# Optimization experiments

Hardware: AMD Instinct MI355X
Metric: run time of the kernel (lower is better)

The kernel has to match this reference:

```python
import jax, jax.numpy as jnp
import numpy as np

K = 3          # kernel size
SH, SW = 2, 1  # stride
PH, PW = 1, 1  # padding


def conv2d(x, w, b, stride, pad):
    y = jax.lax.conv_general_dilated(
        x, w, window_strides=stride,
        padding=[(pad[0], pad[0]), (pad[1], pad[1])],
        dimension_numbers=('NCHW', 'OIHW', 'NCHW'))
    return y + b[None, :, None, None]


def setup_inputs() -> dict:
    key = jax.random.key(0)
    ks = jax.random.split(key, 4)
    x = jax.random.normal(ks[0], (8, 64, 128, 128), jnp.float32)
    # scale offset weights small so sampled offsets are O(1) pixels (exercises
    # the bilinear path without sampling far out of bounds)
    w_offset = jax.random.normal(ks[1], (18, 64, 3, 3), jnp.float32) * 0.02
    b_offset = jnp.zeros((18,), jnp.float32)
    w_mask = jax.random.normal(ks[2], (9, 64, 3, 3), jnp.float32) * 0.05
    b_mask = jnp.zeros((9,), jnp.float32)
    w_conv = jax.random.normal(ks[3], (64, 64, 3, 3), jnp.float32) * (1.0 / 24.0)
    return dict(x=x, w_offset=w_offset, b_offset=b_offset,
                w_mask=w_mask, b_mask=b_mask, w_conv=w_conv)


def _bilinear_gather(x, py, px):
    # x: [B,C,H,W]; py, px: [B,K2,Ho,Wo] float sampling coordinates.
    # Zero-padding outside the image (torchvision deform_conv2d semantics).
    B, C, H, W = x.shape
    y0f = jnp.floor(py)
    x0f = jnp.floor(px)
    dy = py - y0f
    dx = px - x0f
    y0 = y0f.astype(jnp.int32)
    x0 = x0f.astype(jnp.int32)

    def corner(yi, xi, wgt):
        valid = (yi >= 0) & (yi < H) & (xi >= 0) & (xi < W)
        yc = jnp.clip(yi, 0, H - 1)
        xc = jnp.clip(xi, 0, W - 1)
        # per-batch fancy gather -> [B, C, K2, Ho, Wo]
        g = jax.vmap(lambda xb, yb, xbi: xb[:, yb, xbi])(x, yc, xc)
        return g * (wgt * valid)[:, None]

    return (corner(y0,     x0,     (1 - dy) * (1 - dx))
            + corner(y0,     x0 + 1, (1 - dy) * dx)
            + corner(y0 + 1, x0,     dy * (1 - dx))
            + corner(y0 + 1, x0 + 1, dy * dx))


def reference(x, w_offset, b_offset, w_mask, b_mask, w_conv):
    B, C, H, W = x.shape
    offset = conv2d(x, w_offset, b_offset, (SH, SW), (PH, PW))   # [B, 2*K2, Ho, Wo]
    mask = jax.nn.sigmoid(conv2d(x, w_mask, b_mask, (SH, SW), (PH, PW)))  # [B, K2, Ho, Wo]
    Ho, Wo = offset.shape[2], offset.shape[3]
    K2 = K * K
    off = offset.reshape(B, K2, 2, Ho, Wo)
    off_y = off[:, :, 0]   # [B,K2,Ho,Wo]
    off_x = off[:, :, 1]
    ky = (jnp.arange(K2) // K).astype(jnp.float32)
    kx = (jnp.arange(K2) % K).astype(jnp.float32)
    hs = (jnp.arange(Ho) * SH - PH).astype(jnp.float32)
    ws = (jnp.arange(Wo) * SW - PW).astype(jnp.float32)
    py = off_y + ky[None, :, None, None] + hs[None, None, :, None]
    px = off_x + kx[None, :, None, None] + ws[None, None, None, :]
    sampled = _bilinear_gather(x, py, px) * mask[:, None]  # [B,C,K2,Ho,Wo]
    # weighted accumulate over in-channels and kernel taps
    out = jnp.einsum('ock,bckhw->bohw', w_conv.reshape(-1, C, K2), sampled)
    return out
```

## Files before the change

### kernel.cpp

```cpp
#include <hip/hip_runtime.h>
#include <hip/hip_fp16.h>
#include <math.h>

#define BB 8
#define CC 64
#define HH 128
#define WW 128
#define HO 64
#define WO 128
#define OC 64
#define HW (HH * WW)

typedef __attribute__((ext_vector_type(4))) float floatx4;
typedef __attribute__((ext_vector_type(8))) _Float16 half8;

__device__ __forceinline__ unsigned short f2h(float f) {
    __half h = __float2half(f);
    return __builtin_bit_cast(unsigned short, h);
}
__device__ __forceinline__ unsigned int packpair(float a, float b) {
    __half2 h = __floats2half2_rn(a, b);
    return __builtin_bit_cast(unsigned int, h);
}
__device__ __forceinline__ void wave_fence() {
    asm volatile("s_waitcnt lgkmcnt(0)" ::: "memory");
}

__global__ __launch_bounds__(256) void prep(
    const float* __restrict__ x,
    const float* __restrict__ w_off, const float* __restrict__ w_msk,
    const float* __restrict__ w_conv,
    unsigned int* __restrict__ xP,
    unsigned short* __restrict__ Wom, unsigned short* __restrict__ W2)
{
    __shared__ float T[66][65];
    int tid = threadIdx.x, bx = blockIdx.x;
    if (bx < 2048) {
        int wh = bx & 1, b = (bx >> 1) & 7, y = bx >> 4;
        int w0 = wh << 6;
        const float* xb = x + (((size_t)b * CC) * HH + y) * WW + w0;
#pragma unroll
        for (int i = 0; i < 4; ++i) {
            int idx = i * 256 + tid;
            int cch = idx >> 4, f4 = (idx & 15) << 2;
            floatx4 v = *(const floatx4*)(xb + (size_t)cch * HW + f4);
            T[f4 + 0][cch] = v.x;
            T[f4 + 1][cch] = v.y;
            T[f4 + 2][cch] = v.z;
            T[f4 + 3][cch] = v.w;
        }
        if (tid < 64) {
            float e = 0.0f;
            if (w0 + 64 < WW) e = xb[(size_t)tid * HW + 64];
            T[64][tid] = e;
        }
        __syncthreads();
        int c4 = tid & 15;
        int wr = tid >> 4;
        size_t rowbase = (((size_t)b * HH + y) * WW) + w0;
#pragma unroll
        for (int j = 0; j < 4; ++j) {
            int w = 16 * j + wr;
            floatx4 a  = *(const floatx4*)&T[w][4 * c4];
            floatx4 bb = *(const floatx4*)&T[w + 1][4 * c4];
            uint4 d;
            d.x = packpair(a.x, bb.x);
            d.y = packpair(a.y, bb.y);
            d.z = packpair(a.z, bb.z);
            d.w = packpair(a.w, bb.w);
            *(uint4*)(xP + (rowbase + w) * 64 + 4 * c4) = d;
        }
    } else if (bx < 2120) {
        int i = (bx - 2048) * 256 + tid;
        int chn = i / 576, kk = i % 576;
        int xs = kk >> 6, cc = kk & 63;
        float v = 0.0f;
        if (chn < 18)      v = w_off[(chn * CC + cc) * 9 + xs];
        else if (chn < 27) v = w_msk[((chn - 18) * CC + cc) * 9 + xs];
        Wom[i] = f2h(v);
    } else {
        int i = (bx - 2120) * 256 + tid;
        int k = i % 9, cc = (i / 9) % CC, o = i / (CC * 9);
        W2[((size_t)k * OC + o) * CC + cc] = f2h(w_conv[i]);
    }
}

__global__ __launch_bounds__(256) void fused(
    const unsigned int* __restrict__ xP,
    const unsigned short* __restrict__ Wom, const unsigned short* __restrict__ W2,
    const float* __restrict__ b_off, const float* __restrict__ b_msk,
    float* __restrict__ out)
{
    __shared__ __align__(16) char lds[38912];
    int tid = threadIdx.x;
    int lane = tid & 63;
    int wv = __builtin_amdgcn_readfirstlane(tid >> 6);
    char* wb = lds + wv * 9728;
    _Float16* XsH = (_Float16*)wb;
    float* omr = (float*)(wb + 7776);
    uint2* metaRw = (uint2*)wb;
    uint2* metaCw = (uint2*)(wb + 1152);
    char* Sw = wb + 2304;

    int g = blockIdx.x * 4 + wv;
    int b = g >> 9;
    int rem = g & 511;
    int h = rem >> 3;
    int w0 = (rem & 7) << 4;
    int h2 = 2 * h - 1;
    int m16 = lane & 15, q = lane >> 4;

    const unsigned int* xPb_u = xP + (size_t)b * HW * 64;

    for (int u = lane; u < 864; u += 64) {
        int ky = u / 288;
        int rm = u - ky * 288;
        int col = rm >> 4, c4 = rm & 15;
        int hy = h2 + ky, wc = w0 - 1 + col;
        unsigned int lo0 = 0u, lo1 = 0u;
        if ((unsigned)hy < (unsigned)HH && (unsigned)wc < (unsigned)WW) {
            const uint4 gg = *(const uint4*)(xPb_u + ((size_t)hy * WW + wc) * 64 + c4 * 4);
            lo0 = (gg.x & 0xffffu) | (gg.y << 16);
            lo1 = (gg.z & 0xffffu) | (gg.w << 16);
        }
        *(uint2*)(XsH + (ky * 18 + col) * 72 + c4 * 4) = make_uint2(lo0, lo1);
    }
    wave_fence();

    {
        floatx4 a0 = (floatx4){0.f, 0.f, 0.f, 0.f};
        floatx4 a1 = (floatx4){0.f, 0.f, 0.f, 0.f};
        const _Float16* wa0 = (const _Float16*)Wom + m16 * 576 + q * 8;
        const _Float16* wa1 = wa0 + 16 * 576;
#pragma unroll
        for (int t = 0; t < 18; ++t) {
            int xs = t >> 1, ky = xs / 3, kx = xs % 3;
            half8 bf = *(const half8*)(XsH + (ky * 18 + m16 + kx) * 72
                                       + (t & 1) * 32 + q * 8);
            half8 af0 = *(const half8*)(wa0 + t * 32);
            half8 af1 = *(const half8*)(wa1 + t * 32);
            a0 = __builtin_amdgcn_mfma_f32_16x16x32_f16(af0, bf, a0, 0, 0, 0);
            a1 = __builtin_amdgcn_mfma_f32_16x16x32_f16(af1, bf, a1, 0, 0, 0);
        }
#pragma unroll
        for (int r = 0; r < 4; ++r) {
            int c0 = q * 4 + r;
            omr[c0 * 17 + m16] = a0[r];
            if (c0 + 16 < 27) omr[(c0 + 16) * 17 + m16] = a1[r];
        }
    }
    wave_fence();

    for (int u = lane; u < 144; u += 64) {
        int kk = u >> 4, pos = u & 15;
        float offy = omr[(2 * kk) * 17 + pos] + b_off[2 * kk];
        float offx = omr[(2 * kk + 1) * 17 + pos] + b_off[2 * kk + 1];
        float mk = 1.0f / (1.0f + __expf(-(omr[(18 + kk) * 17 + pos] + b_msk[kk])));
        float py = offy + (float)(kk / 3) + (float)h2;
        float px = offx + (float)(kk % 3) + (float)(w0 + pos - 1);

        float y0f = floorf(py), x0f = floorf(px);
        float dy = py - y0f, dx = px - x0f;
        int y0 = (int)y0f, x0 = (int)x0f;
        int y1 = y0 + 1, x1 = x0 + 1;
        bool vy0 = (unsigned)y0 < (unsigned)HH;
        bool vy1 = (unsigned)y1 < (unsigned)HH;
        bool vx0 = (unsigned)x0 < (unsigned)WW;
        bool vx1 = (unsigned)x1 < (unsigned)WW;
        float w00 = (1.0f - dy) * (1.0f - dx) * ((vy0 && vx0) ? mk : 0.0f);
        float w01 = (1.0f - dy) * dx          * ((vy0 && vx1) ? mk : 0.0f);
        float w10 = dy * (1.0f - dx)          * ((vy1 && vx0) ? mk : 0.0f);
        float w11 = dy * dx                   * ((vy1 && vx1) ? mk : 0.0f);
        int xbase = min(max(x0, 0), WW - 2);
        bool s0 = x0 > xbase;
        bool s1 = x1 > xbase;
        float cxA = (s0 ? 0.f : w00) + (s1 ? 0.f : w01);
        float cyA = (s0 ? w00 : 0.f) + (s1 ? w01 : 0.f);
        float cxB = (s0 ? 0.f : w10) + (s1 ? 0.f : w11);
        float cyB = (s0 ? w10 : 0.f) + (s1 ? w11 : 0.f);
        int yc0 = min(max(y0, 0), HH - 1);
        int yc1 = min(max(y1, 0), HH - 1);

        __half2 hA = __floats2half2_rn(cxA, cyA);
        __half2 hB = __floats2half2_rn(cxB, cyB);
        metaCw[u] = make_uint2(__builtin_bit_cast(unsigned int, hA),
                               __builtin_bit_cast(unsigned int, hB));
        metaRw[u] = make_uint2((unsigned)(yc0 * WW + xbase) * 256u,
                               (unsigned)(yc1 * WW + xbase) * 256u);
    }
    wave_fence();

    int p = lane & 31;
    int ph4 = (lane >> 5) << 2;
    unsigned int voffC = 8u * (unsigned)p;
    const char* xPb = (const char*)xPb_u;

    floatx4 acc[4];
#pragma unroll
    for (int m = 0; m < 4; ++m) acc[m] = (floatx4){0.f, 0.f, 0.f, 0.f};

    half8 A[8];
    uint2 Ga0[4], Ga1[4], Gb0[4], Gb1[4];

    auto loadA = [&](int k) {
#pragma unroll
        for (int m = 0; m < 4; ++m)
#pragma unroll
            for (int ks = 0; ks < 2; ++ks)
                A[m * 2 + ks] = *(const half8*)((const _Float16*)W2
                    + ((size_t)(k * OC + m * 16 + m16)) * CC + ks * 32 + q * 8);
    };
    auto issueG = [&](int hhk, uint2 (&G0)[4], uint2 (&G1)[4]) {
        int k = hhk >> 1;
#pragma unroll
        for (int i = 0; i < 4; ++i) {
            int rw = ((hhk & 1) << 3) + ph4 + i;
            uint2 zw = metaRw[k * 16 + rw];
            G0[i] = *(const uint2*)(xPb + (zw.x + voffC));
            G1[i] = *(const uint2*)(xPb + (zw.y + voffC));
        }
    };
    auto blend = [&](int hhk, uint2 (&G0)[4], uint2 (&G1)[4]) {
        int k = hhk >> 1;
#pragma unroll
        for (int i = 0; i < 4; ++i) {
            int rw = ((hhk & 1) << 3) + ph4 + i;
            uint2 cf = metaCw[k * 16 + rw];
            __half2 hA = __builtin_bit_cast(__half2, cf.x);
            __half2 hB = __builtin_bit_cast(__half2, cf.y);
            __half2 t0 = __hfma2(hA, __builtin_bit_cast(__half2, G0[i].x),
                                 __hmul2(hB, __builtin_bit_cast(__half2, G1[i].x)));
            __half2 t1 = __hfma2(hA, __builtin_bit_cast(__half2, G0[i].y),
                                 __hmul2(hB, __builtin_bit_cast(__half2, G1[i].y)));
            __half v0 = __hadd(__low2half(t0), __high2half(t0));
            __half v1 = __hadd(__low2half(t1), __high2half(t1));
            unsigned int d = (unsigned int)__builtin_bit_cast(unsigned short, v0)
                           | ((unsigned int)__builtin_bit_cast(unsigned short, v1) << 16);
            *(unsigned int*)(Sw + rw * 128
                + (((p >> 2) ^ (rw & 7)) * 16 + (p & 3) * 4)) = d;
        }
    };
    auto mfma_tap = [&]() {
        half8 Bf0 = *(const half8*)(Sw + m16 * 128 + ((q ^ (m16 & 7)) * 16));
        half8 Bf1 = *(const half8*)(Sw + m16 * 128 + (((4 + q) ^ (m16 & 7)) * 16));
#pragma unroll
        for (int m = 0; m < 4; ++m) {
            acc[m] = __builtin_amdgcn_mfma_f32_16x16x32_f16(A[m * 2 + 0], Bf0, acc[m], 0, 0, 0);
            acc[m] = __builtin_amdgcn_mfma_f32_16x16x32_f16(A[m * 2 + 1], Bf1, acc[m], 0, 0, 0);
        }
    };

    loadA(0);
    issueG(0, Ga0, Ga1);
#pragma unroll 1
    for (int hh = 0; hh < 18; ++hh) {
        if (hh < 17) {
            if ((hh & 1) == 0) issueG(hh + 1, Gb0, Gb1);
            else               issueG(hh + 1, Ga0, Ga1);
        }
        __builtin_amdgcn_sched_barrier(0);
        if ((hh & 1) == 0) blend(hh, Ga0, Ga1);
        else               blend(hh, Gb0, Gb1);
        if (hh & 1) {
            wave_fence();
            mfma_tap();
            if (hh < 17) loadA((hh >> 1) + 1);
            __builtin_amdgcn_sched_barrier(0);
        }
    }

#pragma unroll
    for (int m = 0; m < 4; ++m)
#pragma unroll
        for (int r = 0; r < 4; ++r) {
            int o = m * 16 + q * 4 + r;
            out[(((size_t)b * OC + o) * HO + h) * WO + w0 + m16] = acc[m][r];
        }
}

extern "C" void kernel_launch(void* const* d_in, const int* in_sizes, int n_in,
                              void* d_out, int out_size, void* d_ws, size_t ws_size,
                              hipStream_t stream)
{
    const float* x      = (const float*)d_in[0];
    const float* w_off  = (const float*)d_in[1];
    const float* b_off  = (const float*)d_in[2];
    const float* w_msk  = (const float*)d_in[3];
    const float* b_msk  = (const float*)d_in[4];
    const float* w_conv = (const float*)d_in[5];
    float* out = (float*)d_out;

    unsigned int* xP = (unsigned int*)d_ws;
    unsigned short* Wom = (unsigned short*)(xP + (size_t)BB * HW * 64);
    unsigned short* W2 = Wom + 32 * 576;

    prep<<<dim3(2264), dim3(256), 0, stream>>>(x, w_off, w_msk, w_conv,
                                               xP, Wom, W2);
    fused<<<dim3(1024), dim3(256), 0, stream>>>(xP, Wom, W2,
                                                b_off, b_msk, out);
}
```

Measured before the change: 168.1 us.

## Use zero-padded NHWC fp16 layout and read offset-conv inputs directly from global

The prep kernel now writes x as a zero-padded (130x130) channel-last fp16 image instead of the paired-column packed layout, halving the intermediate size. The fused kernel drops the per-wave LDS staging of the 3x18 input tile and loads offset-conv operands straight from global memory, relying on padding to remove bounds checks. The bilinear gather now issues four separate corner loads with duplicated half2 coefficients, and the block-to-tile mapping is reordered so batches interleave. Together these cut LDS use and the workspace footprint, at the cost of more, smaller global loads in the gather loop.

```diff
diff --git a/kernel.cpp b/kernel.cpp
--- a/kernel.cpp
+++ b/kernel.cpp
@@ -10,6 +10,9 @@
 #define WO 128
 #define OC 64
 #define HW (HH * WW)
+#define PR 130
+#define PC 130
+#define PLH (PR * PC * 64)
 
 typedef __attribute__((ext_vector_type(4))) float floatx4;
 typedef __attribute__((ext_vector_type(8))) _Float16 half8;
@@ -18,8 +21,12 @@
     __half h = __float2half(f);
     return __builtin_bit_cast(unsigned short, h);
 }
-__device__ __forceinline__ unsigned int packpair(float a, float b) {
+__device__ __forceinline__ unsigned int pack2(float a, float b) {
     __half2 h = __floats2half2_rn(a, b);
+    return __builtin_bit_cast(unsigned int, h);
+}
+__device__ __forceinline__ unsigned int dup2(float a) {
+    __half2 h = __floats2half2_rn(a, a);
     return __builtin_bit_cast(unsigned int, h);
 }
 __device__ __forceinline__ void wave_fence() {
@@ -30,15 +37,16 @@
     const float* __restrict__ x,
     const float* __restrict__ w_off, const float* __restrict__ w_msk,
     const float* __restrict__ w_conv,
-    unsigned int* __restrict__ xP,
+    unsigned short* __restrict__ xH,
     unsigned short* __restrict__ Wom, unsigned short* __restrict__ W2)
 {
     __shared__ float T[66][65];
     int tid = threadIdx.x, bx = blockIdx.x;
     if (bx < 2048) {
-        int wh = bx & 1, b = (bx >> 1) & 7, y = bx >> 4;
+        int b = bx & 7, y = (bx >> 3) & 127, wh = bx >> 10;
         int w0 = wh << 6;
         const float* xb = x + (((size_t)b * CC) * HH + y) * WW + w0;
+        unsigned short* xhb = xH + (size_t)b * PLH;
 #pragma unroll
         for (int i = 0; i < 4; ++i) {
             int idx = i * 256 + tid;
@@ -49,26 +57,24 @@
             T[f4 + 2][cch] = v.z;
             T[f4 + 3][cch] = v.w;
         }
-        if (tid < 64) {
-            float e = 0.0f;
-            if (w0 + 64 < WW) e = xb[(size_t)tid * HW + 64];
-            T[64][tid] = e;
-        }
         __syncthreads();
-        int c4 = tid & 15;
-        int wr = tid >> 4;
-        size_t rowbase = (((size_t)b * HH + y) * WW) + w0;
-#pragma unroll
-        for (int j = 0; j < 4; ++j) {
-            int w = 16 * j + wr;
-            floatx4 a  = *(const floatx4*)&T[w][4 * c4];
-            floatx4 bb = *(const floatx4*)&T[w + 1][4 * c4];
+        int c8 = tid & 7, wr = tid >> 3;
+#pragma unroll
+        for (int j = 0; j < 2; ++j) {
+            int w = j * 32 + wr;
+            floatx4 a = *(const floatx4*)&T[w][8 * c8];
+            floatx4 c = *(const floatx4*)&T[w][8 * c8 + 4];
             uint4 d;
-            d.x = packpair(a.x, bb.x);
-            d.y = packpair(a.y, bb.y);
-            d.z = packpair(a.z, bb.z);
-            d.w = packpair(a.w, bb.w);
-            *(uint4*)(xP + (rowbase + w) * 64 + 4 * c4) = d;
+            d.x = pack2(a.x, a.y);
+            d.y = pack2(a.z, a.w);
+            d.z = pack2(c.x, c.y);
+            d.w = pack2(c.z, c.w);
+            *(uint4*)(xhb + ((size_t)(y + 1) * PC + (w0 + w + 1)) * 64 + 8 * c8) = d;
+        }
+        if (tid < 8) {
+            uint4 z = make_uint4(0u, 0u, 0u, 0u);
+            int pcol = (wh == 0) ? 0 : 129;
+            *(uint4*)(xhb + ((size_t)(y + 1) * PC + pcol) * 64 + 8 * tid) = z;
         }
     } else if (bx < 2120) {
         int i = (bx - 2048) * 256 + tid;
@@ -78,65 +84,58 @@
         if (chn < 18)      v = w_off[(chn * CC + cc) * 9 + xs];
         else if (chn < 27) v = w_msk[((chn - 18) * CC + cc) * 9 + xs];
         Wom[i] = f2h(v);
-    } else {
+    } else if (bx < 2264) {
         int i = (bx - 2120) * 256 + tid;
         int k = i % 9, cc = (i / 9) % CC, o = i / (CC * 9);
         W2[((size_t)k * OC + o) * CC + cc] = f2h(w_conv[i]);
+    } else {
+        int i = (bx - 2264) * 2048 + tid * 8;
+        int b = i / 16640;
+        int r = i - b * 16640;
+        int prow = (r < 8320) ? 0 : 129;
+        int rr = (r < 8320) ? r : r - 8320;
+        uint4 z = make_uint4(0u, 0u, 0u, 0u);
+        *(uint4*)(xH + (size_t)b * PLH + (size_t)prow * PC * 64 + rr) = z;
     }
 }
 
 __global__ __launch_bounds__(256) void fused(
-    const unsigned int* __restrict__ xP,
+    const unsigned short* __restrict__ xH,
     const unsigned short* __restrict__ Wom, const unsigned short* __restrict__ W2,
     const float* __restrict__ b_off, const float* __restrict__ b_msk,
     float* __restrict__ out)
 {
-    __shared__ __align__(16) char lds[38912];
+    __shared__ __align__(16) char lds[22528];
     int tid = threadIdx.x;
     int lane = tid & 63;
     int wv = __builtin_amdgcn_readfirstlane(tid >> 6);
-    char* wb = lds + wv * 9728;
-    _Float16* XsH = (_Float16*)wb;
-    float* omr = (float*)(wb + 7776);
+    char* wb = lds + wv * 5632;
     uint2* metaRw = (uint2*)wb;
-    uint2* metaCw = (uint2*)(wb + 1152);
-    char* Sw = wb + 2304;
-
-    int g = blockIdx.x * 4 + wv;
-    int b = g >> 9;
-    int rem = g & 511;
-    int h = rem >> 3;
-    int w0 = (rem & 7) << 4;
+    uint4* metaCw = (uint4*)(wb + 1152);
+    float* omr = (float*)(wb + 3456);
+    char* Sw = wb + 3456;
+
+    int bx = blockIdx.x;
+    int b = bx & 7;
+    int r2 = bx >> 3;
+    int h = r2 >> 1;
+    int w0 = ((r2 & 1) << 6) + wv * 16;
     int h2 = 2 * h - 1;
     int m16 = lane & 15, q = lane >> 4;
 
-    const unsigned int* xPb_u = xP + (size_t)b * HW * 64;
-
-    for (int u = lane; u < 864; u += 64) {
-        int ky = u / 288;
-        int rm = u - ky * 288;
-        int col = rm >> 4, c4 = rm & 15;
-        int hy = h2 + ky, wc = w0 - 1 + col;
-        unsigned int lo0 = 0u, lo1 = 0u;
-        if ((unsigned)hy < (unsigned)HH && (unsigned)wc < (unsigned)WW) {
-            const uint4 gg = *(const uint4*)(xPb_u + ((size_t)hy * WW + wc) * 64 + c4 * 4);
-            lo0 = (gg.x & 0xffffu) | (gg.y << 16);
-            lo1 = (gg.z & 0xffffu) | (gg.w << 16);
-        }
-        *(uint2*)(XsH + (ky * 18 + col) * 72 + c4 * 4) = make_uint2(lo0, lo1);
-    }
-    wave_fence();
+    const unsigned short* xHb = xH + (size_t)b * PLH;
 
     {
         floatx4 a0 = (floatx4){0.f, 0.f, 0.f, 0.f};
         floatx4 a1 = (floatx4){0.f, 0.f, 0.f, 0.f};
         const _Float16* wa0 = (const _Float16*)Wom + m16 * 576 + q * 8;
         const _Float16* wa1 = wa0 + 16 * 576;
+        const _Float16* xcol = (const _Float16*)xHb + ((size_t)w0 + m16) * 64 + q * 8;
 #pragma unroll
         for (int t = 0; t < 18; ++t) {
             int xs = t >> 1, ky = xs / 3, kx = xs % 3;
-            half8 bf = *(const half8*)(XsH + (ky * 18 + m16 + kx) * 72
-                                       + (t & 1) * 32 + q * 8);
+            half8 bf = *(const half8*)(xcol + ((size_t)(h2 + ky + 1) * PC + kx) * 64
+                                       + (t & 1) * 32);
             half8 af0 = *(const half8*)(wa0 + t * 32);
             half8 af1 = *(const half8*)(wa1 + t * 32);
             a0 = __builtin_amdgcn_mfma_f32_16x16x32_f16(af0, bf, a0, 0, 0, 0);
@@ -181,26 +180,23 @@
         int yc0 = min(max(y0, 0), HH - 1);
         int yc1 = min(max(y1, 0), HH - 1);
 
-        __half2 hA = __floats2half2_rn(cxA, cyA);
-        __half2 hB = __floats2half2_rn(cxB, cyB);
-        metaCw[u] = make_uint2(__builtin_bit_cast(unsigned int, hA),
-                               __builtin_bit_cast(unsigned int, hB));
-        metaRw[u] = make_uint2((unsigned)(yc0 * WW + xbase) * 256u,
-                               (unsigned)(yc1 * WW + xbase) * 256u);
+        metaCw[u] = make_uint4(dup2(cxA), dup2(cyA), dup2(cxB), dup2(cyB));
+        metaRw[u] = make_uint2((unsigned)((yc0 + 1) * PC + xbase + 1) * 128u,
+                               (unsigned)((yc1 + 1) * PC + xbase + 1) * 128u);
     }
     wave_fence();
 
-    int p = lane & 31;
-    int ph4 = (lane >> 5) << 2;
-    unsigned int voffC = 8u * (unsigned)p;
-    const char* xPb = (const char*)xPb_u;
+    int p16 = m16;
+    int pg = q;
+    unsigned int voffC = 8u * (unsigned)p16;
+    const char* xPb = (const char*)xHb;
 
     floatx4 acc[4];
 #pragma unroll
     for (int m = 0; m < 4; ++m) acc[m] = (floatx4){0.f, 0.f, 0.f, 0.f};
 
     half8 A[8];
-    uint2 Ga0[4], Ga1[4], Gb0[4], Gb1[4];
+    uint2 Ga[2][4], Gb[2][4];
 
     auto loadA = [&](int k) {
 #pragma unroll
@@ -210,34 +206,42 @@
                 A[m * 2 + ks] = *(const half8*)((const _Float16*)W2
                     + ((size_t)(k * OC + m * 16 + m16)) * CC + ks * 32 + q * 8);
     };
-    auto issueG = [&](int hhk, uint2 (&G0)[4], uint2 (&G1)[4]) {
+    auto issueG = [&](int hhk, uint2 (&G)[2][4]) {
         int k = hhk >> 1;
 #pragma unroll
-        for (int i = 0; i < 4; ++i) {
-            int rw = ((hhk & 1) << 3) + ph4 + i;
+        for (int grp = 0; grp < 2; ++grp) {
+            int rw = ((hhk & 1) << 3) + grp * 4 + pg;
             uint2 zw = metaRw[k * 16 + rw];
-            G0[i] = *(const uint2*)(xPb + (zw.x + voffC));
-            G1[i] = *(const uint2*)(xPb + (zw.y + voffC));
+            const char* r0 = xPb + (zw.x + voffC);
+            const char* r1 = xPb + (zw.y + voffC);
+            G[grp][0] = *(const uint2*)(r0);
+            G[grp][1] = *(const uint2*)(r0 + 128);
+            G[grp][2] = *(const uint2*)(r1);
+            G[grp][3] = *(const uint2*)(r1 + 128);
         }
     };
-    auto blend = [&](int hhk, uint2 (&G0)[4], uint2 (&G1)[4]) {
+    auto blend = [&](int hhk, uint2 (&G)[2][4]) {
         int k = hhk >> 1;
 #pragma unroll
-        for (int i = 0; i < 4; ++i) {
-            int rw = ((hhk & 1) << 3) + ph4 + i;
-            uint2 cf = metaCw[k * 16 + rw];
-            __half2 hA = __builtin_bit_cast(__half2, cf.x);
-            __half2 hB = __builtin_bit_cast(__half2, cf.y);
-            __half2 t0 = __hfma2(hA, __builtin_bit_cast(__half2, G0[i].x),
-                                 __hmul2(hB, __builtin_bit_cast(__half2, G1[i].x)));
-            __half2 t1 = __hfma2(hA, __builtin_bit_cast(__half2, G0[i].y),
-                                 __hmul2(hB, __builtin_bit_cast(__half2, G1[i].y)));
-            __half v0 = __hadd(__low2half(t0), __high2half(t0));
-            __half v1 = __hadd(__low2half(t1), __high2half(t1));
-            unsigned int d = (unsigned int)__builtin_bit_cast(unsigned short, v0)
-                           | ((unsigned int)__builtin_bit_cast(unsigned short, v1) << 16);
-            *(unsigned int*)(Sw + rw * 128
-                + (((p >> 2) ^ (rw & 7)) * 16 + (p & 3) * 4)) = d;
+        for (int grp = 0; grp < 2; ++grp) {
+            int rw = ((hhk & 1) << 3) + grp * 4 + pg;
+            uint4 cf = metaCw[k * 16 + rw];
+            __half2 cA = __builtin_bit_cast(__half2, cf.x);
+            __half2 cB = __builtin_bit_cast(__half2, cf.y);
+            __half2 cC = __builtin_bit_cast(__half2, cf.z);
+            __half2 cD = __builtin_bit_cast(__half2, cf.w);
+            __half2 lo = __hmul2(cA, __builtin_bit_cast(__half2, G[grp][0].x));
+            lo = __hfma2(cB, __builtin_bit_cast(__half2, G[grp][1].x), lo);
+            lo = __hfma2(cC, __builtin_bit_cast(__half2, G[grp][2].x), lo);
+            lo = __hfma2(cD, __builtin_bit_cast(__half2, G[grp][3].x), lo);
+            __half2 hi = __hmul2(cA, __builtin_bit_cast(__half2, G[grp][0].y));
+            hi = __hfma2(cB, __builtin_bit_cast(__half2, G[grp][1].y), hi);
+            hi = __hfma2(cC, __builtin_bit_cast(__half2, G[grp][2].y), hi);
+            hi = __hfma2(cD, __builtin_bit_cast(__half2, G[grp][3].y), hi);
+            unsigned int soff = (unsigned)(rw * 128
+                + (((p16 >> 1) ^ (rw & 7)) * 16 + (p16 & 1) * 8));
+            *(uint2*)(Sw + soff) = make_uint2(__builtin_bit_cast(unsigned int, lo),
+                                              __builtin_bit_cast(unsigned int, hi));
         }
     };
     auto mfma_tap = [&]() {
@@ -251,16 +255,16 @@
     };
 
     loadA(0);
-    issueG(0, Ga0, Ga1);
+    issueG(0, Ga);
 #pragma unroll 1
     for (int hh = 0; hh < 18; ++hh) {
         if (hh < 17) {
-            if ((hh & 1) == 0) issueG(hh + 1, Gb0, Gb1);
-            else               issueG(hh + 1, Ga0, Ga1);
+            if ((hh & 1) == 0) issueG(hh + 1, Gb);
+            else               issueG(hh + 1, Ga);
         }
         __builtin_amdgcn_sched_barrier(0);
-        if ((hh & 1) == 0) blend(hh, Ga0, Ga1);
-        else               blend(hh, Gb0, Gb1);
+        if ((hh & 1) == 0) blend(hh, Ga);
+        else               blend(hh, Gb);
         if (hh & 1) {
             wave_fence();
             mfma_tap();
@@ -290,12 +294,12 @@
     const float* w_conv = (const float*)d_in[5];
     float* out = (float*)d_out;
 
-    unsigned int* xP = (unsigned int*)d_ws;
-    unsigned short* Wom = (unsigned short*)(xP + (size_t)BB * HW * 64);
+    unsigned short* xH = (unsigned short*)d_ws;
+    unsigned short* Wom = xH + (size_t)BB * PLH;
     unsigned short* W2 = Wom + 32 * 576;
 
-    prep<<<dim3(2264), dim3(256), 0, stream>>>(x, w_off, w_msk, w_conv,
-                                               xP, Wom, W2);
-    fused<<<dim3(1024), dim3(256), 0, stream>>>(xP, Wom, W2,
+    prep<<<dim3(2329), dim3(256), 0, stream>>>(x, w_off, w_msk, w_conv,
+                                               xH, Wom, W2);
+    fused<<<dim3(1024), dim3(256), 0, stream>>>(xH, Wom, W2,
                                                 b_off, b_msk, out);
 }
```

Measured after the change: 164.5 us. -2.1%, faster.
